# Performance work log

Hardware: AMD Instinct MI355X
Metric: run time of the kernel (lower is better)

## Reference

```python
import jax, jax.numpy as jnp
import numpy as np
from jax import lax


def _dw_conv(x, w, dilation):
    # depthwise dilated conv along width; x: [B,H,W,C], w: [1,K,1,C] (HWIO, groups=C)
    return lax.conv_general_dilated(
        x, w,
        window_strides=(1, 1),
        padding='SAME',
        rhs_dilation=(1, dilation),
        dimension_numbers=('NHWC', 'HWIO', 'NHWC'),
        feature_group_count=x.shape[-1])


def setup_inputs() -> dict:
    key = jax.random.key(0)
    kx, k1, k2, k3 = jax.random.split(key, 4)
    B, H, W, C = 16, 21, 4096, 64
    K = 8
    scale = 1.0 / np.sqrt(K)  # keep activations O(1) across stages
    x = jax.random.normal(kx, (B, H, W, C), dtype=jnp.float32)
    w1 = jax.random.normal(k1, (1, K, 1, C), dtype=jnp.float32) * scale
    w2 = jax.random.normal(k2, (1, K, 1, C), dtype=jnp.float32) * scale
    w3 = jax.random.normal(k3, (1, K, 1, C), dtype=jnp.float32) * scale
    return {'x': x, 'w1': w1, 'w2': w2, 'w3': w3}


def reference(x, w1, w2, w3):
    # per-channel Conv2D stack == depthwise conv stack; dilations 1, 2, 4; relu after each
    y = jax.nn.relu(_dw_conv(x, w1, 1))
    y = jax.nn.relu(_dw_conv(y, w2, 2))
    y = jax.nn.relu(_dw_conv(y, w3, 4))
    return y
```

## Files before the change

kernel.cpp:

```cpp
#include <hip/hip_runtime.h>


#define W_DIM   4096
#define C_DIM   64
#define L_CHUNK 256
#define NCHUNK  16
#define NROWS   336
#define WAVES_PER_BLOCK 4

__global__ __launch_bounds__(256, 4)
void splitconv_fused_kernel(const float* __restrict__ x,
                            const float* __restrict__ w1,
                            const float* __restrict__ w2,
                            const float* __restrict__ w3,
                            float* __restrict__ out) {
    const int lane   = threadIdx.x & 63;
    const int waveId = blockIdx.x * WAVES_PER_BLOCK + (threadIdx.x >> 6);
    const int row    = waveId >> 4;
    const int chunk  = waveId & (NCHUNK - 1);
    const int w0     = chunk * L_CHUNK;
    const int c      = lane;

    const float* __restrict__ xrow = x   + (size_t)row * (W_DIM * C_DIM) + c;
    float* __restrict__       orow = out + (size_t)row * (W_DIM * C_DIM) + c;

    float w1r[8], w2r[8], w3r[8];
#pragma unroll
    for (int k = 0; k < 8; ++k) {
        w1r[k] = w1[k * C_DIM + c];
        w2r[k] = w2[k * C_DIM + c];
        w3r[k] = w3[k * C_DIM + c];
    }

    float xf[16], s1f[16], s2f[32];
#pragma unroll
    for (int i = 0; i < 16; ++i) { xf[i] = 0.f; s1f[i] = 0.f; }
#pragma unroll
    for (int i = 0; i < 32; ++i) s2f[i] = 0.f;

    for (int g = 0; g < 10; ++g) {
        const int tbase = w0 - 32 + g * 32;
#pragma unroll
        for (int j = 0; j < 32; ++j) {
            const int t = tbase + j;

            {
                const int z = t + 8;
                float xv = 0.f;
                if (z >= 0 && z < W_DIM && (z - w0) <= L_CHUNK + 24)
                    xv = xrow[(size_t)z * C_DIM];
                xf[(j + 8) & 15] = xv;
            }

            {
                const int v = t - 4;
                float a = 0.f;
#pragma unroll
                for (int k = 0; k < 8; ++k)
                    a = fmaf(xf[(j - 7 + k + 32) & 15], w1r[k], a);
                float s = fmaxf(a, 0.f);
                s1f[(j - 4 + 32) & 15] = (v >= 0 && v < W_DIM) ? s : 0.f;
            }

            {
                const int u = t - 11;
                float a = 0.f;
#pragma unroll
                for (int k = 0; k < 8; ++k)
                    a = fmaf(s1f[(j - 18 + 2 * k + 32) & 15], w2r[k], a);
                float s = fmaxf(a, 0.f);
                s2f[(j - 11 + 32) & 31] = (u >= 0 && u < W_DIM) ? s : 0.f;
            }

            {
                const int wq = t - 25;
                if (wq >= w0 && wq < w0 + L_CHUNK) {
                    float a = 0.f;
#pragma unroll
                    for (int k = 0; k < 8; ++k)
                        a = fmaf(s2f[(j - 39 + 4 * k + 64) & 31], w3r[k], a);
                    orow[(size_t)wq * C_DIM] = fmaxf(a, 0.f);
                }
            }
        }
    }
}

extern "C" void kernel_launch(void* const* d_in, const int* in_sizes, int n_in,
                              void* d_out, int out_size, void* d_ws, size_t ws_size,
                              hipStream_t stream) {
    const float* x  = (const float*)d_in[0];
    const float* w1 = (const float*)d_in[1];
    const float* w2 = (const float*)d_in[2];
    const float* w3 = (const float*)d_in[3];
    float* out = (float*)d_out;

    const int totalWaves = NROWS * NCHUNK;
    const int blocks = totalWaves / WAVES_PER_BLOCK;
    splitconv_fused_kernel<<<blocks, 256, 0, stream>>>(x, w1, w2, w3, out);
}
```

Before: 650.4 us.

## Specialize interior chunks with branch-free peeled loops and remap waves to rows

Interior chunks (1-14) now take a specialized path: the prologue and epilogue groups are peeled, and the main groups run without per-element bounds checks on loads, masks on intermediates, or output predicates. Only edge chunks keep the general guarded loop. The block-to-work mapping also changes so the four waves in a block handle the same chunk of four different rows instead of four consecutive chunks of one row. The intent is to remove per-iteration compare and select overhead in the hot loop, at the cost of larger code and a different memory access locality pattern.

```diff
diff --git a/kernel.cpp b/kernel.cpp
--- a/kernel.cpp
+++ b/kernel.cpp
@@ -8,18 +8,42 @@
 #define NROWS   336
 #define WAVES_PER_BLOCK 4
 
+#define S1_BODY(j) do {                                                     \
+    float a_ = 0.f;                                                         \
+    _Pragma("unroll")                                                       \
+    for (int k = 0; k < 8; ++k)                                             \
+        a_ = fmaf(xf[((j) - 7 + k + 32) & 15], w1r[k], a_);                 \
+    s1f[((j) - 4 + 32) & 15] = fmaxf(a_, 0.f);                              \
+} while (0)
+
+#define S2_BODY(j) do {                                                     \
+    float a_ = 0.f;                                                         \
+    _Pragma("unroll")                                                       \
+    for (int k = 0; k < 8; ++k)                                             \
+        a_ = fmaf(s1f[((j) - 18 + 2 * k + 32) & 15], w2r[k], a_);           \
+    s2f[((j) - 11 + 32) & 31] = fmaxf(a_, 0.f);                             \
+} while (0)
+
+#define S3_STORE(j, dst) do {                                               \
+    float a_ = 0.f;                                                         \
+    _Pragma("unroll")                                                       \
+    for (int k = 0; k < 8; ++k)                                             \
+        a_ = fmaf(s2f[((j) - 39 + 4 * k + 64) & 31], w3r[k], a_);           \
+    (dst) = fmaxf(a_, 0.f);                                                 \
+} while (0)
+
 __global__ __launch_bounds__(256, 4)
 void splitconv_fused_kernel(const float* __restrict__ x,
                             const float* __restrict__ w1,
                             const float* __restrict__ w2,
                             const float* __restrict__ w3,
                             float* __restrict__ out) {
-    const int lane   = threadIdx.x & 63;
-    const int waveId = blockIdx.x * WAVES_PER_BLOCK + (threadIdx.x >> 6);
-    const int row    = waveId >> 4;
-    const int chunk  = waveId & (NCHUNK - 1);
-    const int w0     = chunk * L_CHUNK;
-    const int c      = lane;
+    const int lane  = threadIdx.x & 63;
+    const int wid   = threadIdx.x >> 6;
+    const int chunk = blockIdx.x & (NCHUNK - 1);
+    const int row   = (blockIdx.x >> 4) * WAVES_PER_BLOCK + wid;
+    const int w0    = chunk * L_CHUNK;
+    const int c     = lane;
 
     const float* __restrict__ xrow = x   + (size_t)row * (W_DIM * C_DIM) + c;
     float* __restrict__       orow = out + (size_t)row * (W_DIM * C_DIM) + c;
@@ -38,48 +62,91 @@
 #pragma unroll
     for (int i = 0; i < 32; ++i) s2f[i] = 0.f;
 
-    for (int g = 0; g < 10; ++g) {
-        const int tbase = w0 - 32 + g * 32;
+    if (chunk >= 1 && chunk <= 14) {
+        const float* __restrict__ xp = xrow + (size_t)(w0 - 24) * C_DIM;
+        float* __restrict__       op = orow + (size_t)w0 * C_DIM;
+
 #pragma unroll
         for (int j = 0; j < 32; ++j) {
-            const int t = tbase + j;
+            xf[(j + 8) & 15] = xp[j * C_DIM];
+            if (j >= 15) S1_BODY(j);
+            if (j >= 29) S2_BODY(j);
+        }
+        xp += 32 * C_DIM;
 
-            {
-                const int z = t + 8;
-                float xv = 0.f;
-                if (z >= 0 && z < W_DIM && (z - w0) <= L_CHUNK + 24)
-                    xv = xrow[(size_t)z * C_DIM];
-                xf[(j + 8) & 15] = xv;
+#pragma unroll
+        for (int j = 0; j < 32; ++j) {
+            xf[(j + 8) & 15] = xp[j * C_DIM];
+            S1_BODY(j);
+            S2_BODY(j);
+            if (j >= 25) S3_STORE(j, op[(j - 25) * C_DIM]);
+        }
+        xp += 32 * C_DIM;
+        op += 7 * C_DIM;
+
+#pragma unroll 1
+        for (int g = 2; g <= 8; ++g) {
+#pragma unroll
+            for (int j = 0; j < 32; ++j) {
+                xf[(j + 8) & 15] = xp[j * C_DIM];
+                S1_BODY(j);
+                S2_BODY(j);
+                S3_STORE(j, op[j * C_DIM]);
             }
+            xp += 32 * C_DIM;
+            op += 32 * C_DIM;
+        }
 
-            {
-                const int v = t - 4;
-                float a = 0.f;
 #pragma unroll
-                for (int k = 0; k < 8; ++k)
-                    a = fmaf(xf[(j - 7 + k + 32) & 15], w1r[k], a);
-                float s = fmaxf(a, 0.f);
-                s1f[(j - 4 + 32) & 15] = (v >= 0 && v < W_DIM) ? s : 0.f;
-            }
+        for (int j = 0; j < 32; ++j) {
+            if (j <= 16) xf[(j + 8) & 15] = xp[j * C_DIM];
+            if (j <= 24) { S1_BODY(j); S2_BODY(j); }
+            if (j <  25) S3_STORE(j, op[j * C_DIM]);
+        }
+    } else {
+        for (int g = 0; g < 10; ++g) {
+            const int tbase = w0 - 32 + g * 32;
+#pragma unroll
+            for (int j = 0; j < 32; ++j) {
+                const int t = tbase + j;
 
-            {
-                const int u = t - 11;
-                float a = 0.f;
-#pragma unroll
-                for (int k = 0; k < 8; ++k)
-                    a = fmaf(s1f[(j - 18 + 2 * k + 32) & 15], w2r[k], a);
-                float s = fmaxf(a, 0.f);
-                s2f[(j - 11 + 32) & 31] = (u >= 0 && u < W_DIM) ? s : 0.f;
-            }
+                {
+                    const int z = t + 8;
+                    float xv = 0.f;
+                    if (z >= 0 && z < W_DIM && (z - w0) <= L_CHUNK + 24)
+                        xv = xrow[(size_t)z * C_DIM];
+                    xf[(j + 8) & 15] = xv;
+                }
 
-            {
-                const int wq = t - 25;
-                if (wq >= w0 && wq < w0 + L_CHUNK) {
+                {
+                    const int v = t - 4;
                     float a = 0.f;
 #pragma unroll
                     for (int k = 0; k < 8; ++k)
-                        a = fmaf(s2f[(j - 39 + 4 * k + 64) & 31], w3r[k], a);
-                    orow[(size_t)wq * C_DIM] = fmaxf(a, 0.f);
+                        a = fmaf(xf[(j - 7 + k + 32) & 15], w1r[k], a);
+                    float s = fmaxf(a, 0.f);
+                    s1f[(j - 4 + 32) & 15] = (v >= 0 && v < W_DIM) ? s : 0.f;
+                }
+
+                {
+                    const int u = t - 11;
+                    float a = 0.f;
+#pragma unroll
+                    for (int k = 0; k < 8; ++k)
+                        a = fmaf(s1f[(j - 18 + 2 * k + 32) & 15], w2r[k], a);
+                    float s = fmaxf(a, 0.f);
+                    s2f[(j - 11 + 32) & 31] = (u >= 0 && u < W_DIM) ? s : 0.f;
+                }
+
+                {
+                    const int wq = t - 25;
+                    if (wq >= w0 && wq < w0 + L_CHUNK) {
+                        float a = 0.f;
+#pragma unroll
+                        for (int k = 0; k < 8; ++k)
+                            a = fmaf(s2f[(j - 39 + 4 * k + 64) & 31], w3r[k], a);
+                        orow[(size_t)wq * C_DIM] = fmaxf(a, 0.f);
+                    }
                 }
             }
         }
```

New measurement: 640.8 us. No clear change (-1.5%).
